# Performance work log

Measured on AMD Instinct MI355X. Metric: run time of the kernel, lower is better.

The kernel has to match this reference:

```python
import jax, jax.numpy as jnp
import numpy as np

N = 4096      # (num_domains+1) * batch_size
F_IN = 512    # nfeat
HID = 64      # nhid per head
H = 8         # nheads
ALPHA = 0.2   # leaky-relu negative slope
EDGE_P = 0.01 # adjacency density


def setup_inputs() -> dict:
    key = jax.random.key(0)
    k1, k2, k3, k4 = jax.random.split(key, 4)
    x = jax.random.normal(k1, (N, F_IN), dtype=jnp.float32)
    adj = (jax.random.uniform(k2, (N, N)) < EDGE_P).astype(jnp.float32)
    # ensure self-loops so every row has at least one valid edge for softmax
    adj = jnp.maximum(adj, jnp.eye(N, dtype=jnp.float32))
    W = jax.random.normal(k3, (H, F_IN, HID), dtype=jnp.float32) * 0.1
    a = jax.random.normal(k4, (H, 2 * HID), dtype=jnp.float32) * 0.1
    return {"x": x, "adj": adj, "W": W, "a": a}


def reference(x, adj, W, a):
    # Wh: [H, N, HID] -- per-head linear projection
    Wh = jnp.einsum('nf,hfd->hnd', x, W)
    # additive attention logits: e_ij = leakyrelu(a1.Wh_i + a2.Wh_j)
    e_src = jnp.einsum('hnd,hd->hn', Wh, a[:, :HID])   # [H, N]
    e_dst = jnp.einsum('hnd,hd->hn', Wh, a[:, HID:])   # [H, N]
    e = jax.nn.leaky_relu(e_src[:, :, None] + e_dst[:, None, :], ALPHA)  # [H, N, N]
    e = jnp.where(adj[None] > 0, e, jnp.float32(-9e15))
    att = jax.nn.softmax(e, axis=-1)                    # masked softmax over neighbors
    h = jnp.einsum('hnm,hmd->hnd', att, Wh)             # [H, N, HID]
    h = jax.nn.elu(h)                                   # concat=True -> elu per head
    # concat heads: [N, H*HID]
    return jnp.transpose(h, (1, 0, 2)).reshape(N, H * HID)
```

## Files before the change

### kernel.cpp

```cpp
#include <hip/hip_runtime.h>
#include <hip/hip_bf16.h>
#include <math.h>

#define N_NODES 4096
#define F_IN    512
#define HID     64
#define H       8
#define NJ      512
#define ALPHA   0.2f

typedef __bf16 bf16x8 __attribute__((ext_vector_type(8)));
typedef float  f32x4  __attribute__((ext_vector_type(4)));

#define A_UNITS (N_NODES * F_IN / 4)
#define B_UNITS (NJ * F_IN)

__device__ __forceinline__ void split_bf16(float v, __bf16& hi, __bf16& lo) {
    hi = (__bf16)v;
    lo = (__bf16)(v - (float)hi);
}

__global__ __launch_bounds__(256) void conv_prep(const float* __restrict__ x,
                                                 const float* __restrict__ W,
                                                 __bf16* __restrict__ Ah,
                                                 __bf16* __restrict__ Al,
                                                 __bf16* __restrict__ Bth) {
    int id = blockIdx.x * 256 + threadIdx.x;
    if (id < A_UNITS) {
        float4 v = ((const float4*)x)[id];
        __bf16 h0, h1, h2, h3, l0, l1, l2, l3;
        split_bf16(v.x, h0, l0); split_bf16(v.y, h1, l1);
        split_bf16(v.z, h2, l2); split_bf16(v.w, h3, l3);
        __bf16* ph = Ah + (size_t)id * 4;
        __bf16* pl = Al + (size_t)id * 4;
        ph[0] = h0; ph[1] = h1; ph[2] = h2; ph[3] = h3;
        pl[0] = l0; pl[1] = l1; pl[2] = l2; pl[3] = l3;
    } else {
        int bid = id - A_UNITS;
        if (bid < B_UNITS) {
            int k = bid & (F_IN - 1);
            int j = bid >> 9;
            float v = W[(size_t)(j >> 6) * F_IN * HID + (size_t)k * HID + (j & 63)];
            __bf16 h, l;
            split_bf16(v, h, l);
            Bth[(size_t)j * F_IN + k] = h;
        }
    }
}

__global__ __launch_bounds__(256) void wh_gemm_fused(const __bf16* __restrict__ Ah,
                                                     const __bf16* __restrict__ Al,
                                                     const __bf16* __restrict__ Bth,
                                                     const float* __restrict__ a,
                                                     __bf16* __restrict__ Whb,
                                                     float* __restrict__ esrc,
                                                     float* __restrict__ edst) {
    const int bm = blockIdx.x;
    const int h  = blockIdx.y;
    const int tid  = threadIdx.x;
    const int wave = tid >> 6;
    const int lane = tid & 63;
    const int lm = lane & 15;
    const int lq = lane >> 4;

    __shared__ __align__(16) __bf16 As_h[64][72];
    __shared__ __align__(16) __bf16 As_l[64][72];
    __shared__ __align__(16) __bf16 Bs_h[64][72];

    f32x4 acc[4];
    #pragma unroll
    for (int c = 0; c < 4; c++) acc[c] = (f32x4){0.f, 0.f, 0.f, 0.f};

    for (int k0 = 0; k0 < F_IN; k0 += 64) {
        #pragma unroll
        for (int s = 0; s < 2; s++) {
            int idx = tid + s * 256;
            int m  = idx >> 3;
            int kk = (idx & 7) << 3;
            size_t ga = (size_t)(bm * 64 + m) * F_IN + k0 + kk;
            size_t gb = (size_t)(h * 64 + m) * F_IN + k0 + kk;
            *(uint4*)&As_h[m][kk] = *(const uint4*)(Ah + ga);
            *(uint4*)&As_l[m][kk] = *(const uint4*)(Al + ga);
            *(uint4*)&Bs_h[m][kk] = *(const uint4*)(Bth + gb);
        }
        __syncthreads();

        #pragma unroll
        for (int kh = 0; kh < 2; kh++) {
            bf16x8 afh = *(const bf16x8*)&As_h[wave * 16 + lm][kh * 32 + lq * 8];
            bf16x8 afl = *(const bf16x8*)&As_l[wave * 16 + lm][kh * 32 + lq * 8];
            bf16x8 bh[4];
            #pragma unroll
            for (int c = 0; c < 4; c++) {
                bh[c] = *(const bf16x8*)&Bs_h[c * 16 + lm][kh * 32 + lq * 8];
            }
            #pragma unroll
            for (int c = 0; c < 4; c++) {
                acc[c] = __builtin_amdgcn_mfma_f32_16x16x32_bf16(afh, bh[c], acc[c], 0, 0, 0);
                acc[c] = __builtin_amdgcn_mfma_f32_16x16x32_bf16(afl, bh[c], acc[c], 0, 0, 0);
            }
        }
        __syncthreads();
    }

    float a1c[4], a2c[4];
    #pragma unroll
    for (int c = 0; c < 4; c++) {
        a1c[c] = a[h * 2 * HID + c * 16 + lm];
        a2c[c] = a[h * 2 * HID + HID + c * 16 + lm];
    }

    #pragma unroll
    for (int r = 0; r < 4; r++) {
        int row = bm * 64 + wave * 16 + lq * 4 + r;
        float s1 = 0.f, s2 = 0.f;
        #pragma unroll
        for (int c = 0; c < 4; c++) {
            float v = acc[c][r];
            Whb[(size_t)row * NJ + h * HID + c * 16 + lm] = (__bf16)v;
            s1 += v * a1c[c];
            s2 += v * a2c[c];
        }
        #pragma unroll
        for (int o = 1; o < 16; o <<= 1) {
            s1 += __shfl_xor(s1, o);
            s2 += __shfl_xor(s2, o);
        }
        if (lm == 0) {
            esrc[h * N_NODES + row] = s1;
            edst[h * N_NODES + row] = s2;
        }
    }
}

#define MAXN 128

__global__ __launch_bounds__(256) void gat_attn(const float* __restrict__ adj,
                                                const __bf16* __restrict__ Whb,
                                                const float* __restrict__ esrc,
                                                const float* __restrict__ edst,
                                                float* __restrict__ out) {
    const int i    = blockIdx.x;
    const int tid  = threadIdx.x;
    const int wave = tid >> 6;
    const int lane = tid & 63;
    __shared__ int    nbr[MAXN];
    __shared__ __align__(8)  float2 an[H][MAXN];
    __shared__ float  denom[H];
    __shared__ __align__(16) float4 part[128];
    __shared__ int    cnt;

    if (tid == 0) cnt = 0;
    __syncthreads();

    const unsigned long long lt = (1ull << lane) - 1ull;
    const float4* arow = (const float4*)(adj + (size_t)i * N_NODES);
    float4 q[4];
    #pragma unroll
    for (int cc = 0; cc < 4; cc++) q[cc] = arow[cc * 256 + tid];
    #pragma unroll
    for (int cc = 0; cc < 4; cc++) {
        unsigned long long b0 = __ballot(q[cc].x > 0.f);
        unsigned long long b1 = __ballot(q[cc].y > 0.f);
        unsigned long long b2 = __ballot(q[cc].z > 0.f);
        unsigned long long b3 = __ballot(q[cc].w > 0.f);
        int c0 = __popcll(b0), c1 = __popcll(b1), c2 = __popcll(b2), c3 = __popcll(b3);
        int base = 0;
        if (lane == 0) base = atomicAdd(&cnt, c0 + c1 + c2 + c3);
        base = __shfl(base, 0);
        int col = (cc * 256 + tid) * 4;
        if (q[cc].x > 0.f) nbr[base + __popcll(b0 & lt)] = col;
        base += c0;
        if (q[cc].y > 0.f) nbr[base + __popcll(b1 & lt)] = col + 1;
        base += c1;
        if (q[cc].z > 0.f) nbr[base + __popcll(b2 & lt)] = col + 2;
        base += c2;
        if (q[cc].w > 0.f) nbr[base + __popcll(b3 & lt)] = col + 3;
    }
    __syncthreads();
    const int n = cnt;

    #pragma unroll
    for (int k = 0; k < 2; k++) {
        const int h = wave * 2 + k;
        float es = esrc[h * N_NODES + i];
        float m = -1e30f;
        for (int j = lane; j < n; j += 64) {
            int c = nbr[j];
            float lg = es + edst[h * N_NODES + c];
            lg = lg > 0.f ? lg : ALPHA * lg;
            an[h][j] = make_float2(lg, __int_as_float(c << 10));
            m = fmaxf(m, lg);
        }
        #pragma unroll
        for (int o = 32; o; o >>= 1) m = fmaxf(m, __shfl_xor(m, o));
        float s = 0.f;
        for (int j = lane; j < n; j += 64) {
            float w = __expf(an[h][j].x - m);
            an[h][j].x = w;
            s += w;
        }
        #pragma unroll
        for (int o = 32; o; o >>= 1) s += __shfl_xor(s, o);
        if (lane == 0) denom[h] = s;
    }
    __syncthreads();

    const int qd = tid >> 7;
    const int t  = tid & 127;
    const int h  = t >> 4;
    const char* wp = (const char*)Whb + t * 8;
    float a0 = 0.f, a1 = 0.f, a2 = 0.f, a3 = 0.f;
    #pragma unroll 4
    for (int j = qd; j < n; j += 2) {
        float2 p = an[h][j];
        uint2 u = *(const uint2*)(wp + __float_as_uint(p.y));
        float w = p.x;
        a0 += w * __uint_as_float(u.x << 16);
        a1 += w * __uint_as_float(u.x & 0xffff0000u);
        a2 += w * __uint_as_float(u.y << 16);
        a3 += w * __uint_as_float(u.y & 0xffff0000u);
    }
    if (qd) part[t] = make_float4(a0, a1, a2, a3);
    __syncthreads();
    if (qd == 0) {
        float4 p = part[t];
        a0 += p.x; a1 += p.y; a2 += p.z; a3 += p.w;
        float inv = 1.f / denom[h];
        a0 *= inv; a1 *= inv; a2 *= inv; a3 *= inv;
        a0 = a0 > 0.f ? a0 : expm1f(a0);
        a1 = a1 > 0.f ? a1 : expm1f(a1);
        a2 = a2 > 0.f ? a2 : expm1f(a2);
        a3 = a3 > 0.f ? a3 : expm1f(a3);
        *(float4*)(out + (size_t)i * NJ + t * 4) = make_float4(a0, a1, a2, a3);
    }
}

extern "C" void kernel_launch(void* const* d_in, const int* in_sizes, int n_in,
                              void* d_out, int out_size, void* d_ws, size_t ws_size,
                              hipStream_t stream) {
    const float* x   = (const float*)d_in[0];
    const float* adj = (const float*)d_in[1];
    const float* W   = (const float*)d_in[2];
    const float* a   = (const float*)d_in[3];
    float* out = (float*)d_out;

    float*  esrc = (float*)d_ws;
    float*  edst = esrc + (size_t)H * N_NODES;
    __bf16* Whb  = (__bf16*)(edst + (size_t)H * N_NODES);
    __bf16* Ah   = Whb + (size_t)N_NODES * NJ;
    __bf16* Al   = Ah  + (size_t)N_NODES * F_IN;
    __bf16* Bth  = Al  + (size_t)N_NODES * F_IN;

    conv_prep<<<(A_UNITS + B_UNITS) / 256, 256, 0, stream>>>(x, W, Ah, Al, Bth);

    dim3 g1(N_NODES / 64, H);
    wh_gemm_fused<<<g1, 256, 0, stream>>>(Ah, Al, Bth, a, Whb, esrc, edst);

    gat_attn<<<N_NODES, 256, 0, stream>>>(adj, Whb, esrc, edst, out);
}
```

Before: 132.6 us.

## Fuse x bf16 split into GEMM, remap blocks per XCD, widen attention aggregation

The separate prep kernel that split x into hi/lo bf16 arrays is removed. The GEMM now loads fp32 x directly and does the split in registers, so the intermediate Ah/Al buffers are never written or read back. The GEMM grid becomes 1D and is remapped so that blocks sharing the same x row tile land on the same XCD, aiming at L2 reuse. The attention kernel uses nontemporal loads for adj and stores for out, has each thread aggregate 8 features with 4 neighbour-split groups instead of 4 features with 2, and pads the an array. The cost is redundant conversion of x across the 8 head blocks.

```diff
diff --git a/kernel.cpp b/kernel.cpp
--- a/kernel.cpp
+++ b/kernel.cpp
@@ -12,51 +12,29 @@
 typedef __bf16 bf16x8 __attribute__((ext_vector_type(8)));
 typedef float  f32x4  __attribute__((ext_vector_type(4)));
 
-#define A_UNITS (N_NODES * F_IN / 4)
 #define B_UNITS (NJ * F_IN)
 
-__device__ __forceinline__ void split_bf16(float v, __bf16& hi, __bf16& lo) {
-    hi = (__bf16)v;
-    lo = (__bf16)(v - (float)hi);
-}
-
-__global__ __launch_bounds__(256) void conv_prep(const float* __restrict__ x,
-                                                 const float* __restrict__ W,
-                                                 __bf16* __restrict__ Ah,
-                                                 __bf16* __restrict__ Al,
-                                                 __bf16* __restrict__ Bth) {
-    int id = blockIdx.x * 256 + threadIdx.x;
-    if (id < A_UNITS) {
-        float4 v = ((const float4*)x)[id];
-        __bf16 h0, h1, h2, h3, l0, l1, l2, l3;
-        split_bf16(v.x, h0, l0); split_bf16(v.y, h1, l1);
-        split_bf16(v.z, h2, l2); split_bf16(v.w, h3, l3);
-        __bf16* ph = Ah + (size_t)id * 4;
-        __bf16* pl = Al + (size_t)id * 4;
-        ph[0] = h0; ph[1] = h1; ph[2] = h2; ph[3] = h3;
-        pl[0] = l0; pl[1] = l1; pl[2] = l2; pl[3] = l3;
-    } else {
-        int bid = id - A_UNITS;
-        if (bid < B_UNITS) {
-            int k = bid & (F_IN - 1);
-            int j = bid >> 9;
-            float v = W[(size_t)(j >> 6) * F_IN * HID + (size_t)k * HID + (j & 63)];
-            __bf16 h, l;
-            split_bf16(v, h, l);
-            Bth[(size_t)j * F_IN + k] = h;
-        }
-    }
-}
-
-__global__ __launch_bounds__(256) void wh_gemm_fused(const __bf16* __restrict__ Ah,
-                                                     const __bf16* __restrict__ Al,
+__global__ __launch_bounds__(256) void conv_w(const float* __restrict__ W,
+                                              __bf16* __restrict__ Bth) {
+    int bid = blockIdx.x * 256 + threadIdx.x;
+    int k = bid & (F_IN - 1);
+    int j = bid >> 9;
+    float v = W[(size_t)(j >> 6) * F_IN * HID + (size_t)k * HID + (j & 63)];
+    Bth[(size_t)j * F_IN + k] = (__bf16)v;
+}
+
+__global__ __launch_bounds__(256) void wh_gemm_fused(const float* __restrict__ x,
                                                      const __bf16* __restrict__ Bth,
                                                      const float* __restrict__ a,
                                                      __bf16* __restrict__ Whb,
                                                      float* __restrict__ esrc,
                                                      float* __restrict__ edst) {
-    const int bm = blockIdx.x;
-    const int h  = blockIdx.y;
+    const int bid = blockIdx.x;
+    const int xcd = bid & 7;
+    const int s0  = bid >> 3;
+    const int bm  = xcd * 8 + (s0 >> 3);
+    const int h   = s0 & 7;
+
     const int tid  = threadIdx.x;
     const int wave = tid >> 6;
     const int lane = tid & 63;
@@ -77,11 +55,20 @@
             int idx = tid + s * 256;
             int m  = idx >> 3;
             int kk = (idx & 7) << 3;
-            size_t ga = (size_t)(bm * 64 + m) * F_IN + k0 + kk;
-            size_t gb = (size_t)(h * 64 + m) * F_IN + k0 + kk;
-            *(uint4*)&As_h[m][kk] = *(const uint4*)(Ah + ga);
-            *(uint4*)&As_l[m][kk] = *(const uint4*)(Al + ga);
-            *(uint4*)&Bs_h[m][kk] = *(const uint4*)(Bth + gb);
+            const float4* gp = (const float4*)(x + (size_t)(bm * 64 + m) * F_IN + k0 + kk);
+            float4 v0 = gp[0];
+            float4 v1 = gp[1];
+            float vv[8] = {v0.x, v0.y, v0.z, v0.w, v1.x, v1.y, v1.z, v1.w};
+            bf16x8 hv, lv;
+            #pragma unroll
+            for (int e = 0; e < 8; e++) {
+                __bf16 hi = (__bf16)vv[e];
+                hv[e] = hi;
+                lv[e] = (__bf16)(vv[e] - (float)hi);
+            }
+            *(bf16x8*)&As_h[m][kk] = hv;
+            *(bf16x8*)&As_l[m][kk] = lv;
+            *(uint4*)&Bs_h[m][kk] = *(const uint4*)(Bth + (size_t)(h * 64 + m) * F_IN + k0 + kk);
         }
         __syncthreads();
 
@@ -145,94 +132,113 @@
     const int wave = tid >> 6;
     const int lane = tid & 63;
     __shared__ int    nbr[MAXN];
-    __shared__ __align__(8)  float2 an[H][MAXN];
+    __shared__ __align__(8)  float2 an[H][MAXN + 4];
     __shared__ float  denom[H];
-    __shared__ __align__(16) float4 part[128];
+    __shared__ __align__(16) f32x4 part[3][2][64];
     __shared__ int    cnt;
 
     if (tid == 0) cnt = 0;
     __syncthreads();
 
     const unsigned long long lt = (1ull << lane) - 1ull;
-    const float4* arow = (const float4*)(adj + (size_t)i * N_NODES);
-    float4 q[4];
-    #pragma unroll
-    for (int cc = 0; cc < 4; cc++) q[cc] = arow[cc * 256 + tid];
+    const f32x4* arow = (const f32x4*)(adj + (size_t)i * N_NODES);
+    f32x4 q[4];
+    #pragma unroll
+    for (int cc = 0; cc < 4; cc++) q[cc] = __builtin_nontemporal_load(arow + cc * 256 + tid);
     #pragma unroll
     for (int cc = 0; cc < 4; cc++) {
-        unsigned long long b0 = __ballot(q[cc].x > 0.f);
-        unsigned long long b1 = __ballot(q[cc].y > 0.f);
-        unsigned long long b2 = __ballot(q[cc].z > 0.f);
-        unsigned long long b3 = __ballot(q[cc].w > 0.f);
+        unsigned long long b0 = __ballot(q[cc][0] > 0.f);
+        unsigned long long b1 = __ballot(q[cc][1] > 0.f);
+        unsigned long long b2 = __ballot(q[cc][2] > 0.f);
+        unsigned long long b3 = __ballot(q[cc][3] > 0.f);
         int c0 = __popcll(b0), c1 = __popcll(b1), c2 = __popcll(b2), c3 = __popcll(b3);
         int base = 0;
         if (lane == 0) base = atomicAdd(&cnt, c0 + c1 + c2 + c3);
         base = __shfl(base, 0);
         int col = (cc * 256 + tid) * 4;
-        if (q[cc].x > 0.f) nbr[base + __popcll(b0 & lt)] = col;
+        if (q[cc][0] > 0.f) nbr[base + __popcll(b0 & lt)] = col;
         base += c0;
-        if (q[cc].y > 0.f) nbr[base + __popcll(b1 & lt)] = col + 1;
+        if (q[cc][1] > 0.f) nbr[base + __popcll(b1 & lt)] = col + 1;
         base += c1;
-        if (q[cc].z > 0.f) nbr[base + __popcll(b2 & lt)] = col + 2;
+        if (q[cc][2] > 0.f) nbr[base + __popcll(b2 & lt)] = col + 2;
         base += c2;
-        if (q[cc].w > 0.f) nbr[base + __popcll(b3 & lt)] = col + 3;
+        if (q[cc][3] > 0.f) nbr[base + __popcll(b3 & lt)] = col + 3;
     }
     __syncthreads();
     const int n = cnt;
 
     #pragma unroll
     for (int k = 0; k < 2; k++) {
-        const int h = wave * 2 + k;
-        float es = esrc[h * N_NODES + i];
+        const int hh = wave * 2 + k;
+        float es = esrc[hh * N_NODES + i];
         float m = -1e30f;
         for (int j = lane; j < n; j += 64) {
             int c = nbr[j];
-            float lg = es + edst[h * N_NODES + c];
+            float lg = es + edst[hh * N_NODES + c];
             lg = lg > 0.f ? lg : ALPHA * lg;
-            an[h][j] = make_float2(lg, __int_as_float(c << 10));
+            an[hh][j] = make_float2(lg, __int_as_float(c << 10));
             m = fmaxf(m, lg);
         }
         #pragma unroll
         for (int o = 32; o; o >>= 1) m = fmaxf(m, __shfl_xor(m, o));
         float s = 0.f;
         for (int j = lane; j < n; j += 64) {
-            float w = __expf(an[h][j].x - m);
-            an[h][j].x = w;
+            float w = __expf(an[hh][j].x - m);
+            an[hh][j].x = w;
             s += w;
         }
         #pragma unroll
         for (int o = 32; o; o >>= 1) s += __shfl_xor(s, o);
-        if (lane == 0) denom[h] = s;
-    }
-    __syncthreads();
-
-    const int qd = tid >> 7;
-    const int t  = tid & 127;
-    const int h  = t >> 4;
-    const char* wp = (const char*)Whb + t * 8;
+        if (lane == 0) denom[hh] = s;
+    }
+    __syncthreads();
+
+    const int qd = tid >> 6;
+    const int t  = tid & 63;
+    const int h  = t >> 3;
+    const char* wp = (const char*)Whb + t * 16;
     float a0 = 0.f, a1 = 0.f, a2 = 0.f, a3 = 0.f;
+    float a4 = 0.f, a5 = 0.f, a6 = 0.f, a7 = 0.f;
     #pragma unroll 4
-    for (int j = qd; j < n; j += 2) {
+    for (int j = qd; j < n; j += 4) {
         float2 p = an[h][j];
-        uint2 u = *(const uint2*)(wp + __float_as_uint(p.y));
+        uint4 u = *(const uint4*)(wp + __float_as_uint(p.y));
         float w = p.x;
         a0 += w * __uint_as_float(u.x << 16);
         a1 += w * __uint_as_float(u.x & 0xffff0000u);
         a2 += w * __uint_as_float(u.y << 16);
         a3 += w * __uint_as_float(u.y & 0xffff0000u);
-    }
-    if (qd) part[t] = make_float4(a0, a1, a2, a3);
+        a4 += w * __uint_as_float(u.z << 16);
+        a5 += w * __uint_as_float(u.z & 0xffff0000u);
+        a6 += w * __uint_as_float(u.w << 16);
+        a7 += w * __uint_as_float(u.w & 0xffff0000u);
+    }
+    if (qd) {
+        part[qd - 1][0][t] = (f32x4){a0, a1, a2, a3};
+        part[qd - 1][1][t] = (f32x4){a4, a5, a6, a7};
+    }
     __syncthreads();
     if (qd == 0) {
-        float4 p = part[t];
-        a0 += p.x; a1 += p.y; a2 += p.z; a3 += p.w;
+        f32x4 r0 = (f32x4){a0, a1, a2, a3};
+        f32x4 r1 = (f32x4){a4, a5, a6, a7};
+        #pragma unroll
+        for (int s = 0; s < 3; s++) {
+            r0 += part[s][0][t];
+            r1 += part[s][1][t];
+        }
         float inv = 1.f / denom[h];
-        a0 *= inv; a1 *= inv; a2 *= inv; a3 *= inv;
-        a0 = a0 > 0.f ? a0 : expm1f(a0);
-        a1 = a1 > 0.f ? a1 : expm1f(a1);
-        a2 = a2 > 0.f ? a2 : expm1f(a2);
-        a3 = a3 > 0.f ? a3 : expm1f(a3);
-        *(float4*)(out + (size_t)i * NJ + t * 4) = make_float4(a0, a1, a2, a3);
+        float b[8];
+        #pragma unroll
+        for (int e = 0; e < 4; e++) b[e] = r0[e] * inv;
+        #pragma unroll
+        for (int e = 0; e < 4; e++) b[4 + e] = r1[e] * inv;
+        #pragma unroll
+        for (int e = 0; e < 8; e++) b[e] = b[e] > 0.f ? b[e] : expm1f(b[e]);
+        f32x4 o0 = (f32x4){b[0], b[1], b[2], b[3]};
+        f32x4 o1 = (f32x4){b[4], b[5], b[6], b[7]};
+        f32x4* op = (f32x4*)(out + (size_t)i * NJ + t * 8);
+        __builtin_nontemporal_store(o0, op);
+        __builtin_nontemporal_store(o1, op + 1);
     }
 }
 
@@ -248,14 +254,11 @@
     float*  esrc = (float*)d_ws;
     float*  edst = esrc + (size_t)H * N_NODES;
     __bf16* Whb  = (__bf16*)(edst + (size_t)H * N_NODES);
-    __bf16* Ah   = Whb + (size_t)N_NODES * NJ;
-    __bf16* Al   = Ah  + (size_t)N_NODES * F_IN;
-    __bf16* Bth  = Al  + (size_t)N_NODES * F_IN;
-
-    conv_prep<<<(A_UNITS + B_UNITS) / 256, 256, 0, stream>>>(x, W, Ah, Al, Bth);
-
-    dim3 g1(N_NODES / 64, H);
-    wh_gemm_fused<<<g1, 256, 0, stream>>>(Ah, Al, Bth, a, Whb, esrc, edst);
+    __bf16* Bth  = Whb + (size_t)N_NODES * NJ;
+
+    conv_w<<<B_UNITS / 256, 256, 0, stream>>>(W, Bth);
+
+    wh_gemm_fused<<<512, 256, 0, stream>>>(x, Bth, a, Whb, esrc, edst);
 
     gat_attn<<<N_NODES, 256, 0, stream>>>(adj, Whb, esrc, edst, out);
 }
```

Result: slower. 135.4 us (+2.1%).
